# Kernel tuning notes

Hardware: AMD Instinct MI355X
Metric: run time of the kernel (lower is better)

## Reference

```python
import jax, jax.numpy as jnp
import numpy as np

BIN_SIZE = 128
DIST_MULT = 0.1
CLIP_LOW = 0.0
LN_EPS = 1e-6


def setup_inputs() -> dict:
    key = jax.random.key(0)
    ks = jax.random.split(key, 16)
    B, N, F, DD, MAXB = 8, 12800, 256, 128, 200
    s = 0.05  # ~TF random_normal initializer stddev
    inp = {}
    inp["x"] = jax.random.normal(ks[0], (B, N, F), jnp.float32)
    inp["msk"] = jax.random.uniform(ks[1], (B, N)) < 0.9
    # layernorm params
    inp["ln_g"] = jnp.ones((F,), jnp.float32)
    inp["ln_b"] = jnp.zeros((F,), jnp.float32)
    # ffn_dist: Dense(DD, elu) -> Dense(DD)
    inp["w1"] = jax.random.normal(ks[2], (F, DD), jnp.float32) * s
    inp["b1"] = jax.random.normal(ks[3], (DD,), jnp.float32) * s
    inp["w2"] = jax.random.normal(ks[4], (DD, DD), jnp.float32) * s
    inp["b2"] = jax.random.normal(ks[5], (DD,), jnp.float32) * s
    # LSH random rotations (non-trainable)
    inp["rot"] = jax.random.normal(ks[6], (DD, MAXB // 2), jnp.float32) * s
    # two GHConvDense layers (hidden=F -> output=F)
    inp["theta0"] = jax.random.normal(ks[7], (F, F), jnp.float32) * s
    inp["wh0"] = jax.random.normal(ks[8], (F, F), jnp.float32) * s
    inp["wt0"] = jax.random.normal(ks[9], (F, F), jnp.float32) * s
    inp["bt0"] = jax.random.normal(ks[10], (F,), jnp.float32) * s
    inp["theta1"] = jax.random.normal(ks[11], (F, F), jnp.float32) * s
    inp["wh1"] = jax.random.normal(ks[12], (F, F), jnp.float32) * s
    inp["wt1"] = jax.random.normal(ks[13], (F, F), jnp.float32) * s
    inp["bt1"] = jax.random.normal(ks[14], (F,), jnp.float32) * s
    return inp


def _ghconv(x, adj, mskf, theta, wh, wt, bt):
    # x: [B,nb,bs,F], adj: [B,nb,bs,bs], mskf: [B,nb,bs,1]
    deg = jnp.clip(jnp.sum(jnp.abs(adj), axis=-1), 0.0, 1000.0)  # [B,nb,bs]
    norm = ((deg + 1e-6) ** -0.5)[..., None] * mskf
    f_hom = jnp.matmul(x * mskf, theta) * mskf
    f_hom = jnp.matmul(adj, f_hom * norm) * norm
    f_het = jnp.matmul(x * mskf, wh)
    gate = jax.nn.sigmoid(jnp.matmul(x, wt) + bt)
    out = gate * f_hom + (1.0 - gate) * f_het
    return jax.nn.elu(out) * mskf


def _forward(x, msk, ln_g, ln_b, w1, b1, w2, b2, rot,
             theta0, wh0, wt0, bt0, theta1, wh1, wt1, bt1):
    B, N, F = x.shape
    nbins = N // BIN_SIZE
    # layernorm
    mu = jnp.mean(x, axis=-1, keepdims=True)
    var = jnp.mean((x - mu) ** 2, axis=-1, keepdims=True)
    xn = (x - mu) * jax.lax.rsqrt(var + LN_EPS) * ln_g + ln_b
    # ffn_dist
    xd = jnp.matmul(jax.nn.elu(jnp.matmul(xn, w1) + b1), w2) + b2  # [B,N,DD]
    # LSH binning
    mul = jnp.matmul(xd, rot[:, : nbins // 2])
    cmul = jnp.concatenate([mul, -mul], axis=-1)  # [B,N,nbins]
    bin_idx = jnp.argmax(cmul, axis=-1) + jnp.where(~msk, nbins - 1, 0)
    bins_split = jnp.argsort(bin_idx, axis=-1).reshape(B, nbins, BIN_SIZE)
    flat = bins_split.reshape(B, N)
    # gather into bins
    xd_b = jnp.take_along_axis(xd, flat[:, :, None], axis=1).reshape(B, nbins, BIN_SIZE, -1)
    x_b = jnp.take_along_axis(xn, flat[:, :, None], axis=1).reshape(B, nbins, BIN_SIZE, F)
    mskf = msk.astype(x.dtype)[:, :, None]
    m_b = jnp.take_along_axis(mskf, flat[:, :, None], axis=1).reshape(B, nbins, BIN_SIZE, 1)
    # pairwise gaussian kernel within bins
    na = jnp.sum(xd_b * xd_b, axis=-1)
    D2 = na[..., :, None] - 2.0 * jnp.einsum("bnie,bnje->bnij", xd_b, xd_b) + na[..., None, :]
    dm = jnp.exp(-DIST_MULT * jnp.sqrt(jnp.maximum(D2, 1e-6)))
    dm = jnp.clip(dm, CLIP_LOW, 1.0)
    m = m_b[..., 0]
    dm = dm * m[:, :, :, None] * m[:, :, None, :]
    # graph convs
    x_b = _ghconv(x_b, dm, m_b, theta0, wh0, wt0, bt0)
    x_b = _ghconv(x_b, dm, m_b, theta1, wh1, wt1, bt1)
    # reverse LSH scatter
    pts = x_b.reshape(B, N, F)
    x_enc = jnp.zeros((B, N, F), pts.dtype).at[jnp.arange(B)[:, None], flat].set(pts)
    return x_enc


def reference(x, msk, ln_g, ln_b, w1, b1, w2, b2, rot,
              theta0, wh0, wt0, bt0, theta1, wh1, wt1, bt1):
    return _forward(x, msk, ln_g, ln_b, w1, b1, w2, b2, rot,
                    theta0, wh0, wt0, bt0, theta1, wh1, wt1, bt1)
```

## Files before the change

kernel.cpp:

```cpp
#include <hip/hip_runtime.h>
#include <math.h>

#define BB 8
#define NN 12800
#define FF 256
#define DDIM 128
#define NBINS 100
#define BSIZE 128
#define NROT 50
#define NIDS 199
#define PTS (BB*NN)

#define OFF_OUT0 ((size_t)157286400)
#define OFF_DMB  ((size_t)209715200)
#define OFF_WB   ((size_t)235929600)
#define OFF_NORM ((size_t)236716032)
#define OFF_MF   ((size_t)237125632)
#define OFF_BIN  ((size_t)237535232)
#define OFF_FLAT ((size_t)237944832)
#define OFF_MSKI ((size_t)238354432)
#define OFF_HIST ((size_t)238764032)
#define OFF_OFFS ((size_t)239400832)
#define OFF_FLAG ((size_t)240037632)
#define OFF_CNT  ((size_t)240037696)
#define OFF_LIST ((size_t)240037760)
#define OFF_W1H  ((size_t)240447360)
#define OFF_W1L  ((size_t)240512896)
#define OFF_W2H  ((size_t)240578432)
#define OFF_W2L  ((size_t)240611200)
#define OFF_RH   ((size_t)240643968)
#define OFF_RL   ((size_t)240660352)
#define HISTBYTES (8*100*199*4)

using short8  = __attribute__((ext_vector_type(8))) short;
using floatx4 = __attribute__((ext_vector_type(4))) float;

__device__ __forceinline__ ushort f2b(float f) {
    unsigned u = __float_as_uint(f);
    unsigned r = (u + 0x7FFFu + ((u >> 16) & 1u)) >> 16;
    return (ushort)r;
}
__device__ __forceinline__ float b2f(ushort h) {
    return __uint_as_float(((unsigned)h) << 16);
}
__device__ __forceinline__ uint4 pack8(const ushort* o) {
    uint4 u;
    u.x = (unsigned)o[0] | ((unsigned)o[1] << 16);
    u.y = (unsigned)o[2] | ((unsigned)o[3] << 16);
    u.z = (unsigned)o[4] | ((unsigned)o[5] << 16);
    u.w = (unsigned)o[6] | ((unsigned)o[7] << 16);
    return u;
}

__global__ void k_maskflag(const int* mi, int* flag) {
    __shared__ int notInt, notFloat;
    if (threadIdx.x == 0) { notInt = 0; notFloat = 0; }
    __syncthreads();
    int v = mi[threadIdx.x];
    if (v != 0 && v != 1) atomicOr(&notInt, 1);
    if (v != 0 && v != 0x3F800000) atomicOr(&notFloat, 1);
    __syncthreads();
    if (threadIdx.x == 0) flag[0] = (!notInt) ? 0 : ((!notFloat) ? 2 : 1);
}

__global__ void k_masknorm(const void* msk, const int* flag, int* mski) {
    int i = blockIdx.x * blockDim.x + threadIdx.x;
    if (i >= PTS) return;
    int f = flag[0];
    int v;
    if (f == 0)      v = ((const int*)msk)[i] != 0;
    else if (f == 2) v = ((const float*)msk)[i] != 0.0f;
    else             v = ((const unsigned char*)msk)[i] != 0;
    mski[i] = v;
}

__global__ __launch_bounds__(256) void k_wprep(
    const float* s0, const float* s1, const float* s2,
    const float* s3, const float* s4, const float* s5,
    ushort* d0, ushort* d1, ushort* d2, ushort* d3, ushort* d4, ushort* d5)
{
    __shared__ float Ls[64 * 65];
    const float* src; ushort* dst;
    switch (blockIdx.y) {
        case 0: src = s0; dst = d0; break;
        case 1: src = s1; dst = d1; break;
        case 2: src = s2; dst = d2; break;
        case 3: src = s3; dst = d3; break;
        case 4: src = s4; dst = d4; break;
        default: src = s5; dst = d5; break;
    }
    int t = blockIdx.x;
    int kb = (t & 3) * 64, nb = (t >> 2) * 64;
    int tid = threadIdx.x;
    for (int q = 0; q < 4; ++q) {
        int g = q * 256 + tid;
        int kl = g >> 4, f4 = g & 15;
        float4 v = *(const float4*)(src + (size_t)(kb + kl) * 256 + nb + f4 * 4);
        Ls[kl * 65 + f4 * 4 + 0] = v.x;
        Ls[kl * 65 + f4 * 4 + 1] = v.y;
        Ls[kl * 65 + f4 * 4 + 2] = v.z;
        Ls[kl * 65 + f4 * 4 + 3] = v.w;
    }
    __syncthreads();
    for (int q = 0; q < 2; ++q) {
        int g = q * 256 + tid;
        int nl = g >> 3, wg = g & 7;
        ushort o[8];
        #pragma unroll
        for (int c = 0; c < 8; ++c) o[c] = f2b(Ls[(wg * 8 + c) * 65 + nl]);
        *(uint4*)(dst + (size_t)(nb + nl) * 256 + kb + wg * 8) = pack8(o);
    }
}

__global__ __launch_bounds__(256) void k_wsplit(const float* __restrict__ src, int K, int N,
                                               int srcN, int nvalid,
                                               ushort* __restrict__ dh, ushort* __restrict__ dl) {
    __shared__ float Ls[64 * 65];
    int tilesN = N >> 6;
    int kb = (blockIdx.x / tilesN) * 64, nb = (blockIdx.x % tilesN) * 64;
    int tid = threadIdx.x;
    for (int q = 0; q < 4; ++q) {
        int g = q * 256 + tid;
        int kl = g >> 4, c4 = (g & 15) * 4;
        #pragma unroll
        for (int j = 0; j < 4; ++j) {
            int n = nb + c4 + j;
            float v = (n < nvalid) ? src[(size_t)(kb + kl) * srcN + n] : 0.f;
            Ls[kl * 65 + c4 + j] = v;
        }
    }
    __syncthreads();
    for (int q = 0; q < 2; ++q) {
        int g = q * 256 + tid;
        int nl = g >> 3, wg = g & 7;
        ushort oh[8], ol[8];
        #pragma unroll
        for (int c = 0; c < 8; ++c) {
            float v = Ls[(wg * 8 + c) * 65 + nl];
            ushort h = f2b(v);
            oh[c] = h;
            ol[c] = f2b(v - b2f(h));
        }
        *(uint4*)(dh + (size_t)(nb + nl) * K + kb + wg * 8) = pack8(oh);
        *(uint4*)(dl + (size_t)(nb + nl) * K + kb + wg * 8) = pack8(ol);
    }
}

__device__ __forceinline__ void stage_async(const ushort* __restrict__ src, size_t pitch,
                                            const int* __restrict__ rowmap, int rowbase, size_t kbase,
                                            ushort* lds, int nrows, int tid) {
    int lane = tid & 63, wid = tid >> 6;
    int total = nrows * 8;
    for (int b0 = 0; b0 < total; b0 += 512) {
        int g = b0 + wid * 64 + lane;
        int row = g >> 3;
        int ck = (g & 7) ^ (row & 7);
        size_t srow = rowmap ? (size_t)rowmap[rowbase + row] : (size_t)(rowbase + row);
        const ushort* gp = src + srow * pitch + kbase + ck * 8;
        ushort* lp = lds + (size_t)(b0 + wid * 64) * 8;
        __builtin_amdgcn_global_load_lds(
            (const __attribute__((address_space(1))) unsigned int*)gp,
            (__attribute__((address_space(3))) unsigned int*)lp, 16, 0, 0);
    }
}

__device__ __forceinline__ short8 frag_ld(const ushort* lds, int row, int kc, int lane) {
    int w0 = (kc * 16 + ((lane >> 4) << 2)) ^ ((row & 7) << 2);
    return *(const short8*)((const char*)lds + row * 128 + w0 * 4);
}

__global__ __launch_bounds__(512, 4) void k_stage1(
    const float* __restrict__ x, const float* __restrict__ g, const float* __restrict__ be,
    const float* __restrict__ b1, const float* __restrict__ b2,
    const ushort* __restrict__ w1h, const ushort* __restrict__ w1l,
    const ushort* __restrict__ w2h, const ushort* __restrict__ w2l,
    const ushort* __restrict__ rth, const ushort* __restrict__ rtl,
    const int* __restrict__ mski,
    ushort* __restrict__ xn_out, float* __restrict__ xd_out, int* __restrict__ bin_out,
    int* __restrict__ fixlist, int* __restrict__ fixcnt)
{
    __shared__ ushort lXh[4 * 2048];
    __shared__ ushort lXl[4 * 2048];
    __shared__ ushort lWh[8192];
    __shared__ ushort lWl[8192];
    int tid = threadIdx.x, lane = tid & 63, wid = tid >> 6;
    int base = blockIdx.x * 32;
    int l15 = lane & 15;
    int r4 = (lane >> 4) * 4;

    stage_async(w1h, 256, nullptr, 0, 0, lWh, 128, tid);
    stage_async(w1l, 256, nullptr, 0, 0, lWl, 128, tid);

    {
        int row = tid >> 4, sub = tid & 15;
        const float* xr = x + (size_t)(base + row) * FF + sub * 16;
        float v[16];
        float s = 0.f;
        #pragma unroll
        for (int q = 0; q < 4; ++q) {
            float4 f = *(const float4*)(xr + q * 4);
            v[q*4+0] = f.x; v[q*4+1] = f.y; v[q*4+2] = f.z; v[q*4+3] = f.w;
            s += f.x + f.y + f.z + f.w;
        }
        s += __shfl_xor(s, 1, 16); s += __shfl_xor(s, 2, 16);
        s += __shfl_xor(s, 4, 16); s += __shfl_xor(s, 8, 16);
        float mu = s * (1.f / 256.f);
        float s2 = 0.f;
        #pragma unroll
        for (int q = 0; q < 16; ++q) { float d = v[q] - mu; s2 += d * d; }
        s2 += __shfl_xor(s2, 1, 16); s2 += __shfl_xor(s2, 2, 16);
        s2 += __shfl_xor(s2, 4, 16); s2 += __shfl_xor(s2, 8, 16);
        float rs = 1.0f / sqrtf(s2 * (1.f / 256.f) + 1e-6f);
        ushort* xo = xn_out + (size_t)(base + row) * FF + sub * 16;
        #pragma unroll
        for (int j = 0; j < 2; ++j) {
            int i0 = sub * 16 + j * 8;
            float4 g0 = *(const float4*)(g + i0);
            float4 g1 = *(const float4*)(g + i0 + 4);
            float4 e0 = *(const float4*)(be + i0);
            float4 e1 = *(const float4*)(be + i0 + 4);
            float gv[8] = {g0.x,g0.y,g0.z,g0.w,g1.x,g1.y,g1.z,g1.w};
            float ev[8] = {e0.x,e0.y,e0.z,e0.w,e1.x,e1.y,e1.z,e1.w};
            ushort hh[8], ll[8];
            #pragma unroll
            for (int c = 0; c < 8; ++c) {
                float xv = (v[j*8+c] - mu) * rs * gv[c] + ev[c];
                ushort h = f2b(xv);
                hh[c] = h;
                ll[c] = f2b(xv - b2f(h));
            }
            uint4 uh = pack8(hh), ul = pack8(ll);
            *(uint4*)(xo + j * 8) = uh;
            int kb = i0 >> 6;
            int wg = (i0 & 63) >> 3;
            int w0 = (wg * 4) ^ ((row & 7) << 2);
            *(uint4*)((char*)lXh + kb * 4096 + row * 128 + w0 * 4) = uh;
            *(uint4*)((char*)lXl + kb * 4096 + row * 128 + w0 * 4) = ul;
        }
    }
    __syncthreads();

    int mg = wid >> 2, ng = wid & 3;
    int wm = mg * 16, wn = ng * 32;
    floatx4 zf = {0.f, 0.f, 0.f, 0.f};

    floatx4 acc[2];
    acc[0] = zf; acc[1] = zf;
    for (int kb = 0; kb < 4; ++kb) {
        #pragma unroll
        for (int kc = 0; kc < 2; ++kc) {
            short8 ah, al, bh[2], bl[2];
            ah = frag_ld(lXh + kb * 2048, wm + l15, kc, lane);
            al = frag_ld(lXl + kb * 2048, wm + l15, kc, lane);
            #pragma unroll
            for (int n = 0; n < 2; n++) {
                bh[n] = frag_ld(lWh, wn + n * 16 + l15, kc, lane);
                bl[n] = frag_ld(lWl, wn + n * 16 + l15, kc, lane);
            }
            #pragma unroll
            for (int n = 0; n < 2; n++) {
                acc[n] = __builtin_amdgcn_mfma_f32_16x16x32_bf16(ah, bh[n], acc[n], 0, 0, 0);
                acc[n] = __builtin_amdgcn_mfma_f32_16x16x32_bf16(ah, bl[n], acc[n], 0, 0, 0);
                acc[n] = __builtin_amdgcn_mfma_f32_16x16x32_bf16(al, bh[n], acc[n], 0, 0, 0);
            }
        }
        __syncthreads();
        if (kb < 3) {
            stage_async(w1h, 256, nullptr, 0, (size_t)(kb + 1) * 64, lWh, 128, tid);
            stage_async(w1l, 256, nullptr, 0, (size_t)(kb + 1) * 64, lWl, 128, tid);
            __syncthreads();
        }
    }
    stage_async(w2h, 128, nullptr, 0, 0, lWh, 128, tid);
    stage_async(w2l, 128, nullptr, 0, 0, lWl, 128, tid);
    {
        #pragma unroll
        for (int n = 0; n < 2; n++) {
            int cg = wn + n * 16 + l15;
            float b1v = b1[cg];
            int slab = cg >> 6, c64 = cg & 63;
            int wg = c64 >> 3, e = c64 & 7;
            #pragma unroll
            for (int i = 0; i < 4; i++) {
                int r = wm + r4 + i;
                float hv = acc[n][i] + b1v;
                hv = (hv > 0.f) ? hv : expm1f(hv);
                ushort h = f2b(hv);
                int w0 = (wg * 4) ^ ((r & 7) << 2);
                int idx = slab * 2048 + r * 64 + w0 * 2 + e;
                lXh[idx] = h;
                lXl[idx] = f2b(hv - b2f(h));
            }
        }
    }
    __syncthreads();

    floatx4 acc2[2];
    acc2[0] = zf; acc2[1] = zf;
    for (int kb = 0; kb < 2; ++kb) {
        #pragma unroll
        for (int kc = 0; kc < 2; ++kc) {
            short8 ah, al, bh[2], bl[2];
            ah = frag_ld(lXh + kb * 2048, wm + l15, kc, lane);
            al = frag_ld(lXl + kb * 2048, wm + l15, kc, lane);
            #pragma unroll
            for (int n = 0; n < 2; n++) {
                bh[n] = frag_ld(lWh, wn + n * 16 + l15, kc, lane);
                bl[n] = frag_ld(lWl, wn + n * 16 + l15, kc, lane);
            }
            #pragma unroll
            for (int n = 0; n < 2; n++) {
                acc2[n] = __builtin_amdgcn_mfma_f32_16x16x32_bf16(ah, bh[n], acc2[n], 0, 0, 0);
                acc2[n] = __builtin_amdgcn_mfma_f32_16x16x32_bf16(ah, bl[n], acc2[n], 0, 0, 0);
                acc2[n] = __builtin_amdgcn_mfma_f32_16x16x32_bf16(al, bh[n], acc2[n], 0, 0, 0);
            }
        }
        __syncthreads();
        if (kb == 0) {
            stage_async(w2h, 128, nullptr, 0, 64, lWh, 128, tid);
            stage_async(w2l, 128, nullptr, 0, 64, lWl, 128, tid);
            __syncthreads();
        }
    }
    stage_async(rth, 128, nullptr, 0, 0, lWh, 64, tid);
    stage_async(rtl, 128, nullptr, 0, 0, lWl, 64, tid);
    stage_async(rth, 128, nullptr, 0, 64, lWh + 4096, 64, tid);
    stage_async(rtl, 128, nullptr, 0, 64, lWl + 4096, 64, tid);
    {
        #pragma unroll
        for (int n = 0; n < 2; n++) {
            int cg = wn + n * 16 + l15;
            float b2v = b2[cg];
            int slab = 2 + (cg >> 6), c64 = cg & 63;
            int wg = c64 >> 3, e = c64 & 7;
            #pragma unroll
            for (int i = 0; i < 4; i++) {
                int r = wm + r4 + i;
                float xv = acc2[n][i] + b2v;
                xd_out[(size_t)(base + r) * DDIM + cg] = xv;
                ushort h = f2b(xv);
                int w0 = (wg * 4) ^ ((r & 7) << 2);
                int idx = slab * 2048 + r * 64 + w0 * 2 + e;
                lXh[idx] = h;
                lXl[idx] = f2b(xv - b2f(h));
            }
        }
    }
    __syncthreads();

    floatx4 acc3 = zf;
    int wn3 = ng * 16;
    for (int kb = 0; kb < 2; ++kb) {
        #pragma unroll
        for (int kc = 0; kc < 2; ++kc) {
            short8 ah, al, bh, bl;
            ah = frag_ld(lXh + (2 + kb) * 2048, wm + l15, kc, lane);
            al = frag_ld(lXl + (2 + kb) * 2048, wm + l15, kc, lane);
            bh = frag_ld(lWh + kb * 4096, wn3 + l15, kc, lane);
            bl = frag_ld(lWl + kb * 4096, wn3 + l15, kc, lane);
            acc3 = __builtin_amdgcn_mfma_f32_16x16x32_bf16(ah, bh, acc3, 0, 0, 0);
            acc3 = __builtin_amdgcn_mfma_f32_16x16x32_bf16(ah, bl, acc3, 0, 0, 0);
            acc3 = __builtin_amdgcn_mfma_f32_16x16x32_bf16(al, bh, acc3, 0, 0, 0);
        }
    }
    __syncthreads();
    float* lMul = (float*)lXh;
    {
        #pragma unroll
        for (int i = 0; i < 4; i++) {
            int r = wm + r4 + i;
            lMul[r * 65 + wn3 + l15] = acc3[i];
        }
    }
    __syncthreads();

    {
        int p = tid >> 4, q = tid & 15;
        float v1 = -1e30f, v2 = -1e30f; int i1 = 1 << 29;
        #pragma unroll
        for (int j = 0; j < 4; ++j) {
            int c = q * 4 + j;
            if (c < 50) {
                float m = lMul[p * 65 + c];
                float wv, lv; int wi, li;
                if (m >= 0.f) { wv = m; wi = c; lv = -m; li = 50 + c; }
                else          { wv = -m; wi = 50 + c; lv = m; li = c; }
                if (wv > v1 || (wv == v1 && wi < i1)) { v2 = v1; v1 = wv; i1 = wi; }
                else if (wv > v2) v2 = wv;
                if (lv > v1 || (lv == v1 && li < i1)) { v2 = v1; v1 = lv; i1 = li; }
                else if (lv > v2) v2 = lv;
            }
        }
        #pragma unroll
        for (int off = 1; off < 16; off <<= 1) {
            float o1 = __shfl_xor(v1, off, 16);
            int   oi = __shfl_xor(i1, off, 16);
            float o2 = __shfl_xor(v2, off, 16);
            bool take = (o1 > v1) || (o1 == v1 && oi < i1);
            float small = take ? v1 : o1;
            if (take) { v1 = o1; i1 = oi; }
            v2 = fmaxf(fmaxf(v2, o2), small);
        }
        if (q == 0) {
            int pt = base + p;
            bin_out[pt] = i1 + (mski[pt] ? 0 : (NBINS - 1));
            float tau = 3e-4f + 1.5e-3f * v1;
            if (v1 - v2 < tau) {
                int pos = atomicAdd(fixcnt, 1);
                fixlist[pos] = pt;
            }
        }
    }
}

__global__ __launch_bounds__(64) void k_fixup(
    const float* __restrict__ x, const float* __restrict__ g, const float* __restrict__ be,
    const float* __restrict__ w1, const float* __restrict__ b1,
    const float* __restrict__ w2, const float* __restrict__ b2,
    const float* __restrict__ rot, const int* __restrict__ mski,
    const int* __restrict__ fixlist, const int* __restrict__ fixcnt,
    int* __restrict__ bin_out)
{
    __shared__ double xn_s[256];
    __shared__ double h_s[128];
    __shared__ double xd_s[128];
    int lane = threadIdx.x;
    int n = fixcnt[0];
    for (int e = blockIdx.x; e < n; e += gridDim.x) {
        int pt = fixlist[e];
        const float* xr = x + (size_t)pt * FF;
        double s = 0.0, xv[4];
        #pragma unroll
        for (int q = 0; q < 4; q++) { xv[q] = (double)xr[lane + q * 64]; s += xv[q]; }
        #pragma unroll
        for (int off = 1; off < 64; off <<= 1) s += __shfl_xor(s, off, 64);
        double mu = s * (1.0 / 256.0);
        double s2 = 0.0;
        #pragma unroll
        for (int q = 0; q < 4; q++) { double d = xv[q] - mu; s2 += d * d; }
        #pragma unroll
        for (int off = 1; off < 64; off <<= 1) s2 += __shfl_xor(s2, off, 64);
        double rs = 1.0 / sqrt(s2 * (1.0 / 256.0) + 1e-6);
        #pragma unroll
        for (int q = 0; q < 4; q++) {
            int i = lane + q * 64;
            xn_s[i] = (xv[q] - mu) * rs * (double)g[i] + (double)be[i];
        }
        __syncthreads();
        #pragma unroll
        for (int q = 0; q < 2; q++) {
            int j = lane + q * 64;
            double a0 = 0.0, a1 = 0.0;
            for (int k = 0; k < FF; k += 2) {
                a0 += xn_s[k] * (double)w1[k * DDIM + j];
                a1 += xn_s[k + 1] * (double)w1[(k + 1) * DDIM + j];
            }
            double a = (double)b1[j] + a0 + a1;
            h_s[j] = (a > 0.0) ? a : expm1(a);
        }
        __syncthreads();
        #pragma unroll
        for (int q = 0; q < 2; q++) {
            int j = lane + q * 64;
            double a0 = 0.0, a1 = 0.0;
            for (int k = 0; k < DDIM; k += 2) {
                a0 += h_s[k] * (double)w2[k * DDIM + j];
                a1 += h_s[k + 1] * (double)w2[(k + 1) * DDIM + j];
            }
            xd_s[j] = (double)b2[j] + a0 + a1;
        }
        __syncthreads();
        double v; int idx;
        if (lane < NROT) {
            double m = 0.0;
            for (int k = 0; k < DDIM; k++) m += xd_s[k] * (double)rot[k * 100 + lane];
            if (m >= 0.0) { v = m; idx = lane; } else { v = -m; idx = 50 + lane; }
        } else { v = -1e300; idx = 1 << 29; }
        #pragma unroll
        for (int off = 1; off < 64; off <<= 1) {
            double ov = __shfl_xor(v, off, 64);
            int oi = __shfl_xor(idx, off, 64);
            if (ov > v || (ov == v && oi < idx)) { v = ov; idx = oi; }
        }
        if (lane == 0) bin_out[pt] = idx + (mski[pt] ? 0 : (NBINS - 1));
        __syncthreads();
    }
}

__global__ void k_count(const int* __restrict__ bin, int* __restrict__ hist) {
    int c = blockIdx.x % 100, b = blockIdx.x / 100;
    int t = threadIdx.x;
    int v = bin[b * NN + c * BSIZE + t];
    atomicAdd(&hist[(b * 100 + c) * NIDS + v], 1);
}

__global__ void k_offsets(const int* __restrict__ hist, int* __restrict__ offs) {
    __shared__ int tot[NIDS];
    __shared__ int start[NIDS];
    int b = blockIdx.x, v = threadIdx.x;
    if (v < NIDS) {
        int s = 0;
        for (int c = 0; c < 100; c++) s += hist[(b * 100 + c) * NIDS + v];
        tot[v] = s;
    }
    __syncthreads();
    if (threadIdx.x == 0) {
        int run = 0;
        for (int i = 0; i < NIDS; i++) { start[i] = run; run += tot[i]; }
    }
    __syncthreads();
    if (v < NIDS) {
        int run = start[v];
        for (int c = 0; c < 100; c++) {
            offs[(b * 100 + c) * NIDS + v] = run;
            run += hist[(b * 100 + c) * NIDS + v];
        }
    }
}

__global__ void k_scatter(const int* __restrict__ bin, const int* __restrict__ offs,
                          const int* __restrict__ mski, int* __restrict__ flat,
                          float* __restrict__ mf) {
    __shared__ int sv[BSIZE];
    int c = blockIdx.x % 100, b = blockIdx.x / 100;
    int t = threadIdx.x;
    int n = c * BSIZE + t;
    int v = bin[b * NN + n];
    sv[t] = v;
    __syncthreads();
    int rank = 0;
    for (int u = 0; u < t; u++) rank += (sv[u] == v);
    int r = offs[(b * 100 + c) * NIDS + v] + rank;
    flat[b * NN + r] = b * NN + n;
    mf[b * NN + r] = mski[b * NN + n] ? 1.0f : 0.0f;
}

__global__ __launch_bounds__(256) void k_dm(const float* __restrict__ xd, const int* __restrict__ flat,
                                            const float* __restrict__ mf, ushort* __restrict__ dmb,
                                            float* __restrict__ norm) {
    __shared__ float Xs[128 * 64];
    __shared__ float na[128];
    __shared__ float ml[128];
    __shared__ float ps[128 * 16];
    int g = blockIdx.x, tid = threadIdx.x;
    int tx = tid & 15, ty = tid >> 4;
    int rowbase = g * 128;
    if (tid < 128) ml[tid] = mf[rowbase + tid];
    float acc[8][8];
    #pragma unroll
    for (int i = 0; i < 8; i++)
        #pragma unroll
        for (int j = 0; j < 8; j++) acc[i][j] = 0.f;
    float nap[8];
    #pragma unroll
    for (int j = 0; j < 8; j++) nap[j] = 0.f;

    for (int kh = 0; kh < 2; ++kh) {
        __syncthreads();
        for (int q = 0; q < 8; ++q) {
            int gg = q * 256 + tid;
            int row = gg >> 4, f4 = gg & 15;
            int srow = flat[rowbase + row];
            float4 v = *(const float4*)(xd + (size_t)srow * DDIM + kh * 64 + f4 * 4);
            int f4s = f4 ^ ((row >> 3) & 7);
            *(float4*)(Xs + row * 64 + f4s * 4) = v;
        }
        __syncthreads();
        for (int k4 = 0; k4 < 16; ++k4) {
            int sa = (k4 ^ (ty & 7)) << 2;
            int sb = (k4 ^ (tx & 7)) << 2;
            float4 av[8], bv[8];
            #pragma unroll
            for (int i = 0; i < 8; i++) av[i] = *(const float4*)(Xs + (ty * 8 + i) * 64 + sa);
            #pragma unroll
            for (int j = 0; j < 8; j++) bv[j] = *(const float4*)(Xs + (tx * 8 + j) * 64 + sb);
            if (ty == 0) {
                #pragma unroll
                for (int j = 0; j < 8; j++)
                    nap[j] += bv[j].x * bv[j].x + bv[j].y * bv[j].y + bv[j].z * bv[j].z + bv[j].w * bv[j].w;
            }
            #pragma unroll
            for (int i = 0; i < 8; i++)
                #pragma unroll
                for (int j = 0; j < 8; j++)
                    acc[i][j] += av[i].x * bv[j].x + av[i].y * bv[j].y + av[i].z * bv[j].z + av[i].w * bv[j].w;
        }
    }
    if (ty == 0) {
        #pragma unroll
        for (int j = 0; j < 8; j++) na[tx * 8 + j] = nap[j];
    }
    __syncthreads();
    #pragma unroll
    for (int i = 0; i < 8; ++i) {
        int r = ty * 8 + i;
        float nai = na[r], mi = ml[r];
        float rs = 0.f;
        ushort o[8];
        #pragma unroll
        for (int j = 0; j < 8; ++j) {
            int c = tx * 8 + j;
            float D2 = nai - 2.f * acc[i][j] + na[c];
            float dv = expf(-0.1f * sqrtf(fmaxf(D2, 1e-6f)));
            dv *= mi * ml[c];
            rs += dv;
            o[j] = f2b(dv);
        }
        *(uint4*)(dmb + (size_t)g * 16384 + r * 128 + tx * 8) = pack8(o);
        ps[r * 16 + tx] = rs;
    }
    __syncthreads();
    if (tid < 128) {
        float deg = 0.f;
        for (int t2 = 0; t2 < 16; ++t2) deg += ps[tid * 16 + t2];
        deg = fminf(deg, 1000.0f);
        float nv = 1.0f / sqrtf(deg + 1e-6f);
        norm[rowbase + tid] = nv * ml[tid];
    }
}

template<int LAYER>
__global__ __launch_bounds__(512, 4) void k_layer(
    const ushort* __restrict__ A, const int* __restrict__ rowmap,
    const ushort* __restrict__ ThT, const ushort* __restrict__ WhT, const ushort* __restrict__ WtT,
    const float* __restrict__ bt, const ushort* __restrict__ dmb,
    const float* __restrict__ norm, const float* __restrict__ mf,
    ushort* __restrict__ outb, float* __restrict__ outf, const int* __restrict__ flatscat)
{
    __shared__ char smem[81920];
    ushort* lAbuf = (ushort*)smem;
    ushort* lB    = (ushort*)(smem + 32768);
    ushort* lT    = (ushort*)smem;
    ushort* ldm   = (ushort*)(smem + 32768);

    int tid = threadIdx.x, lane = tid & 63, wid = tid >> 6;
    int bid = blockIdx.x;
    int grp = bid >> 5, within = bid & 31;
    int nh = within >> 3, g = grp * 8 + (within & 7);
    int rowbase = g * 128, nbase = nh * 64;
    int l15 = lane & 15;
    int r4 = (lane >> 4) * 4;
    int wm = (wid >> 1) * 32, wn = (wid & 1) * 32;
    const ushort* dmg = dmb + (size_t)g * 16384;
    floatx4 zf = {0.f, 0.f, 0.f, 0.f};

    stage_async(A, 256, rowmap, rowbase, 0, lAbuf, 128, tid);
    stage_async(ThT, 256, nullptr, nbase, 0, lB + 0 * 4096, 64, tid);
    stage_async(WhT, 256, nullptr, nbase, 0, lB + 2 * 4096, 64, tid);
    stage_async(WtT, 256, nullptr, nbase, 0, lB + 4 * 4096, 64, tid);
    __syncthreads();

    floatx4 accT[2][2], accH[2][2], accG[2][2];
    #pragma unroll
    for (int m = 0; m < 2; m++)
        #pragma unroll
        for (int n = 0; n < 2; n++) { accT[m][n] = zf; accH[m][n] = zf; accG[m][n] = zf; }
    for (int kb = 0; kb < 4; ++kb) {
        if (kb < 3) {
            int pp = (kb + 1) & 1;
            stage_async(A, 256, rowmap, rowbase, (size_t)(kb + 1) * 64, lAbuf + pp * 8192, 128, tid);
            stage_async(ThT, 256, nullptr, nbase, (size_t)(kb + 1) * 64, lB + (0 + pp) * 4096, 64, tid);
            stage_async(WhT, 256, nullptr, nbase, (size_t)(kb + 1) * 64, lB + (2 + pp) * 4096, 64, tid);
            stage_async(WtT, 256, nullptr, nbase, (size_t)(kb + 1) * 64, lB + (4 + pp) * 4096, 64, tid);
        }
        const ushort* lA = lAbuf + (kb & 1) * 8192;
        const ushort* sTh = lB + (0 + (kb & 1)) * 4096;
        const ushort* sWh = lB + (2 + (kb & 1)) * 4096;
        const ushort* sWt = lB + (4 + (kb & 1)) * 4096;
        #pragma unroll
        for (int kc = 0; kc < 2; ++kc) {
            short8 a[2], bt_[2], bh_[2], bg_[2];
            #pragma unroll
            for (int m = 0; m < 2; m++) a[m] = frag_ld(lA, wm + m * 16 + l15, kc, lane);
            #pragma unroll
            for (int n = 0; n < 2; n++) {
                bt_[n] = frag_ld(sTh, wn + n * 16 + l15, kc, lane);
                bh_[n] = frag_ld(sWh, wn + n * 16 + l15, kc, lane);
                bg_[n] = frag_ld(sWt, wn + n * 16 + l15, kc, lane);
            }
            #pragma unroll
            for (int m = 0; m < 2; m++)
                #pragma unroll
                for (int n = 0; n < 2; n++) {
                    accT[m][n] = __builtin_amdgcn_mfma_f32_16x16x32_bf16(a[m], bt_[n], accT[m][n], 0, 0, 0);
                    accH[m][n] = __builtin_amdgcn_mfma_f32_16x16x32_bf16(a[m], bh_[n], accH[m][n], 0, 0, 0);
                    accG[m][n] = __builtin_amdgcn_mfma_f32_16x16x32_bf16(a[m], bg_[n], accG[m][n], 0, 0, 0);
                }
        }
        __syncthreads();
    }

    stage_async(dmg, 128, nullptr, 0, 0, ldm, 128, tid);
    stage_async(dmg, 128, nullptr, 0, 64, ldm + 8192, 128, tid);

    {
        #pragma unroll
        for (int m = 0; m < 2; m++) {
            float4 nv = *(const float4*)(norm + rowbase + wm + m * 16 + r4);
            float nvv[4] = {nv.x, nv.y, nv.z, nv.w};
            int jloc0 = wm + m * 16 + r4;
            int jb = jloc0 >> 6, jj = jloc0 & 63;
            #pragma unroll
            for (int n = 0; n < 2; n++) {
                int cloc = wn + n * 16 + l15;
                char* bp = (char*)(lT + jb * 4096) + cloc * 128;
                int cx = (cloc & 7) << 2;
                ushort t0 = f2b(accT[m][n][0] * nvv[0]);
                ushort t1 = f2b(accT[m][n][1] * nvv[1]);
                ushort t2 = f2b(accT[m][n][2] * nvv[2]);
                ushort t3 = f2b(accT[m][n][3] * nvv[3]);
                *(unsigned*)(bp + ((((jj >> 1) + 0) ^ cx) << 2)) = (unsigned)t0 | ((unsigned)t1 << 16);
                *(unsigned*)(bp + ((((jj >> 1) + 1) ^ cx) << 2)) = (unsigned)t2 | ((unsigned)t3 << 16);
            }
        }
    }
    __syncthreads();

    floatx4 accFH[2][2];
    #pragma unroll
    for (int m = 0; m < 2; m++) { accFH[m][0] = zf; accFH[m][1] = zf; }
    for (int kb = 0; kb < 2; ++kb) {
        #pragma unroll
        for (int kc = 0; kc < 2; ++kc) {
            short8 a[2], b[2];
            #pragma unroll
            for (int m = 0; m < 2; m++) a[m] = frag_ld(ldm + kb * 8192, wm + m * 16 + l15, kc, lane);
            #pragma unroll
            for (int n = 0; n < 2; n++) b[n] = frag_ld(lT + kb * 4096, wn + n * 16 + l15, kc, lane);
            #pragma unroll
            for (int m = 0; m < 2; m++)
                #pragma unroll
                for (int n = 0; n < 2; n++)
                    accFH[m][n] = __builtin_amdgcn_mfma_f32_16x16x32_bf16(a[m], b[n], accFH[m][n], 0, 0, 0);
        }
    }
    __syncthreads();

    for (int m = 0; m < 2; m++) {
        int r0l = wm + m * 16 + r4;
        int r0g = rowbase + r0l;
        float4 mv = *(const float4*)(mf + r0g);
        float4 nv = *(const float4*)(norm + r0g);
        float mvv[4] = {mv.x, mv.y, mv.z, mv.w};
        float nvv[4] = {nv.x, nv.y, nv.z, nv.w};
        float vals[2][4];
        #pragma unroll
        for (int n = 0; n < 2; n++) {
            int cg = nbase + wn + n * 16 + l15;
            float btc = bt[cg];
            #pragma unroll
            for (int i = 0; i < 4; i++) {
                float gate = 1.f / (1.f + expf(-(accG[m][n][i] + btc)));
                float fh = accFH[m][n][i] * nvv[i];
                float het = mvv[i] * accH[m][n][i];
                float o = gate * fh + (1.f - gate) * het;
                o = (o > 0.f) ? o : expm1f(o);
                vals[n][i] = o * mvv[i];
            }
        }
        if (LAYER == 0) {
            ushort* Ls = (ushort*)smem;
            int bbase = wid * 512;
            #pragma unroll
            for (int n = 0; n < 2; n++)
                #pragma unroll
                for (int i = 0; i < 4; i++)
                    Ls[bbase + (r4 + i) * 32 + n * 16 + l15] = f2b(vals[n][i]);
            __builtin_amdgcn_s_waitcnt(0);
            #pragma unroll
            for (int it = 0; it < 2; ++it) {
                int lr = (lane >> 3) + it * 8;
                int lc4 = (lane & 7) * 4;
                ushort4 tv = *(const ushort4*)(Ls + bbase + lr * 32 + lc4);
                int rg = rowbase + wm + m * 16 + lr;
                *(ushort4*)(outb + (size_t)rg * 256 + nbase + wn + lc4) = tv;
            }
        } else {
            float* Ls = (float*)smem;
            int bbase = wid * 512;
            #pragma unroll
            for (int n = 0; n < 2; n++)
                #pragma unroll
                for (int i = 0; i < 4; i++)
                    Ls[bbase + (r4 + i) * 32 + n * 16 + l15] = vals[n][i];
            __builtin_amdgcn_s_waitcnt(0);
            #pragma unroll
            for (int it = 0; it < 2; ++it) {
                int lr = (lane >> 3) + it * 8;
                int lc4 = (lane & 7) * 4;
                float4 tv = *(const float4*)(Ls + bbase + lr * 32 + lc4);
                int rg = rowbase + wm + m * 16 + lr;
                int dst = flatscat[rg];
                *(float4*)(outf + (size_t)dst * 256 + nbase + wn + lc4) = tv;
            }
        }
    }
}

extern "C" void kernel_launch(void* const* d_in, const int* in_sizes, int n_in,
                              void* d_out, int out_size, void* d_ws, size_t ws_size,
                              hipStream_t stream) {
    const float* x    = (const float*)d_in[0];
    const void*  msk  = d_in[1];
    const float* ln_g = (const float*)d_in[2];
    const float* ln_b = (const float*)d_in[3];
    const float* w1   = (const float*)d_in[4];
    const float* b1   = (const float*)d_in[5];
    const float* w2   = (const float*)d_in[6];
    const float* b2   = (const float*)d_in[7];
    const float* rot  = (const float*)d_in[8];
    const float* th0  = (const float*)d_in[9];
    const float* wh0  = (const float*)d_in[10];
    const float* wt0  = (const float*)d_in[11];
    const float* bt0  = (const float*)d_in[12];
    const float* th1  = (const float*)d_in[13];
    const float* wh1  = (const float*)d_in[14];
    const float* wt1  = (const float*)d_in[15];
    const float* bt1  = (const float*)d_in[16];

    char* ws = (char*)d_ws;
    ushort* out0 = (ushort*)(ws + OFF_OUT0);
    ushort* dmb  = (ushort*)(ws + OFF_DMB);
    ushort* wb   = (ushort*)(ws + OFF_WB);
    ushort* wbth0 = wb + 0 * 65536;
    ushort* wbwh0 = wb + 1 * 65536;
    ushort* wbwt0 = wb + 2 * 65536;
    ushort* wbth1 = wb + 3 * 65536;
    ushort* wbwh1 = wb + 4 * 65536;
    ushort* wbwt1 = wb + 5 * 65536;
    float* norm = (float*)(ws + OFF_NORM);
    float* mf   = (float*)(ws + OFF_MF);
    int*   bin  = (int*)(ws + OFF_BIN);
    int*   flat = (int*)(ws + OFF_FLAT);
    int*   mski = (int*)(ws + OFF_MSKI);
    int*   hist = (int*)(ws + OFF_HIST);
    int*   offs = (int*)(ws + OFF_OFFS);
    int*   flag = (int*)(ws + OFF_FLAG);
    int*   fixcnt = (int*)(ws + OFF_CNT);
    int*   fixlist = (int*)(ws + OFF_LIST);
    ushort* w1h = (ushort*)(ws + OFF_W1H);
    ushort* w1l = (ushort*)(ws + OFF_W1L);
    ushort* w2h = (ushort*)(ws + OFF_W2H);
    ushort* w2l = (ushort*)(ws + OFF_W2L);
    ushort* rth = (ushort*)(ws + OFF_RH);
    ushort* rtl = (ushort*)(ws + OFF_RL);
    float*  xd  = (float*)d_out;
    ushort* xnb = (ushort*)((char*)d_out + (size_t)PTS * DDIM * 4);

    hipMemsetAsync(hist, 0, HISTBYTES, stream);
    hipMemsetAsync(fixcnt, 0, 4, stream);
    k_maskflag<<<1, 256, 0, stream>>>((const int*)msk, flag);
    k_masknorm<<<PTS / 256, 256, 0, stream>>>(msk, flag, mski);
    k_wprep<<<dim3(16, 6), 256, 0, stream>>>(th0, wh0, wt0, th1, wh1, wt1,
                                             wbth0, wbwh0, wbwt0, wbth1, wbwh1, wbwt1);
    k_wsplit<<<8, 256, 0, stream>>>(w1, 256, 128, 128, 128, w1h, w1l);
    k_wsplit<<<4, 256, 0, stream>>>(w2, 128, 128, 128, 128, w2h, w2l);
    k_wsplit<<<2, 256, 0, stream>>>(rot, 128, 64, 100, 50, rth, rtl);
    k_stage1<<<PTS / 32, 512, 0, stream>>>(x, ln_g, ln_b, b1, b2,
                                           w1h, w1l, w2h, w2l, rth, rtl, mski,
                                           xnb, xd, bin, fixlist, fixcnt);
    k_fixup<<<4096, 64, 0, stream>>>(x, ln_g, ln_b, w1, b1, w2, b2, rot, mski,
                                     fixlist, fixcnt, bin);
    k_count<<<800, 128, 0, stream>>>(bin, hist);
    k_offsets<<<8, 256, 0, stream>>>(hist, offs);
    k_scatter<<<800, 128, 0, stream>>>(bin, offs, mski, flat, mf);
    k_dm<<<800, 256, 0, stream>>>(xd, flat, mf, dmb, norm);
    k_layer<0><<<3200, 512, 0, stream>>>(xnb, flat, wbth0, wbwh0, wbwt0, bt0,
                                         dmb, norm, mf, out0, nullptr, nullptr);
    k_layer<1><<<3200, 512, 0, stream>>>(out0, nullptr, wbth1, wbwh1, wbwt1, bt1,
                                         dmb, norm, mf, nullptr, (float*)d_out, flat);
}
```

Baseline: 439.8 us.

## Compute pairwise bin distances with split-bf16 MFMA instead of fp32 FMA

The pairwise Gram matrix inside each bin moves from a scalar fp32 outer-product loop to MFMA bf16 instructions using a hi/lo split (three MFMAs per tile) for near-fp32 accuracy. To feed it, stage1 now writes the distance features as separate hi and lo bf16 arrays instead of fp32, and the gather uses async global-to-LDS loads. The output tile is staged through padded LDS and written out in coalesced chunks, with the row-sum reduction done by shuffles. Dropping the small low*low term introduces slight precision loss in the distances.

```diff
diff --git a/kernel.cpp b/kernel.cpp
--- a/kernel.cpp
+++ b/kernel.cpp
@@ -176,8 +176,8 @@
     const ushort* __restrict__ w2h, const ushort* __restrict__ w2l,
     const ushort* __restrict__ rth, const ushort* __restrict__ rtl,
     const int* __restrict__ mski,
-    ushort* __restrict__ xn_out, float* __restrict__ xd_out, int* __restrict__ bin_out,
-    int* __restrict__ fixlist, int* __restrict__ fixcnt)
+    ushort* __restrict__ xn_out, ushort* __restrict__ xdh_out, ushort* __restrict__ xdl_out,
+    int* __restrict__ bin_out, int* __restrict__ fixlist, int* __restrict__ fixcnt)
 {
     __shared__ ushort lXh[4 * 2048];
     __shared__ ushort lXl[4 * 2048];
@@ -337,12 +337,15 @@
             for (int i = 0; i < 4; i++) {
                 int r = wm + r4 + i;
                 float xv = acc2[n][i] + b2v;
-                xd_out[(size_t)(base + r) * DDIM + cg] = xv;
                 ushort h = f2b(xv);
+                ushort lo = f2b(xv - b2f(h));
+                size_t go = (size_t)(base + r) * DDIM + cg;
+                xdh_out[go] = h;
+                xdl_out[go] = lo;
                 int w0 = (wg * 4) ^ ((r & 7) << 2);
                 int idx = slab * 2048 + r * 64 + w0 * 2 + e;
                 lXh[idx] = h;
-                lXl[idx] = f2b(xv - b2f(h));
+                lXl[idx] = lo;
             }
         }
     }
@@ -535,87 +538,125 @@
     mf[b * NN + r] = mski[b * NN + n] ? 1.0f : 0.0f;
 }
 
-__global__ __launch_bounds__(256) void k_dm(const float* __restrict__ xd, const int* __restrict__ flat,
-                                            const float* __restrict__ mf, ushort* __restrict__ dmb,
-                                            float* __restrict__ norm) {
-    __shared__ float Xs[128 * 64];
+__global__ __launch_bounds__(512, 4) void k_dm(const ushort* __restrict__ xdh, const ushort* __restrict__ xdl,
+                                               const int* __restrict__ flat, const float* __restrict__ mf,
+                                               ushort* __restrict__ dmb, float* __restrict__ norm) {
+    __shared__ ushort lX[32768];
     __shared__ float na[128];
     __shared__ float ml[128];
-    __shared__ float ps[128 * 16];
-    int g = blockIdx.x, tid = threadIdx.x;
-    int tx = tid & 15, ty = tid >> 4;
+    __shared__ float ps[512];
+    int tid = threadIdx.x, lane = tid & 63, wid = tid >> 6;
+    int g = blockIdx.x;
     int rowbase = g * 128;
+    int l15 = lane & 15;
+    int r4 = (lane >> 4) * 4;
+    int mg = wid >> 2, ng = wid & 3;
+    int wm = mg * 64, wn = ng * 32;
+    floatx4 zf = {0.f, 0.f, 0.f, 0.f};
+
+    stage_async(xdh, 128, flat, rowbase, 0, lX, 128, tid);
+    stage_async(xdh, 128, flat, rowbase, 64, lX + 8192, 128, tid);
+    stage_async(xdl, 128, flat, rowbase, 0, lX + 16384, 128, tid);
+    stage_async(xdl, 128, flat, rowbase, 64, lX + 24576, 128, tid);
     if (tid < 128) ml[tid] = mf[rowbase + tid];
-    float acc[8][8];
+    __syncthreads();
+
+    {
+        int row = tid >> 2, part = tid & 3;
+        float s = 0.f;
+        #pragma unroll
+        for (int kb = 0; kb < 2; ++kb) {
+            const ushort* ph = lX + kb * 8192 + row * 64 + part * 16;
+            #pragma unroll
+            for (int q = 0; q < 2; ++q) {
+                uint4 uh = *(const uint4*)(ph + q * 8);
+                uint4 ul = *(const uint4*)(ph + 16384 + q * 8);
+                const unsigned* wh_ = (const unsigned*)&uh;
+                const unsigned* wl_ = (const unsigned*)&ul;
+                #pragma unroll
+                for (int w = 0; w < 4; ++w) {
+                    float x0 = b2f((ushort)(wh_[w] & 0xFFFFu)) + b2f((ushort)(wl_[w] & 0xFFFFu));
+                    float x1 = b2f((ushort)(wh_[w] >> 16)) + b2f((ushort)(wl_[w] >> 16));
+                    s = fmaf(x0, x0, s);
+                    s = fmaf(x1, x1, s);
+                }
+            }
+        }
+        s += __shfl_xor(s, 1, 4);
+        s += __shfl_xor(s, 2, 4);
+        if (part == 0) na[row] = s;
+    }
+
+    floatx4 acc[4][2];
     #pragma unroll
-    for (int i = 0; i < 8; i++)
-        #pragma unroll
-        for (int j = 0; j < 8; j++) acc[i][j] = 0.f;
-    float nap[8];
+    for (int m = 0; m < 4; m++) { acc[m][0] = zf; acc[m][1] = zf; }
+    for (int kb = 0; kb < 2; ++kb) {
+        #pragma unroll
+        for (int kc = 0; kc < 2; ++kc) {
+            short8 ah[4], al[4], bh[2], bl[2];
+            #pragma unroll
+            for (int m = 0; m < 4; m++) {
+                ah[m] = frag_ld(lX + kb * 8192, wm + m * 16 + l15, kc, lane);
+                al[m] = frag_ld(lX + 16384 + kb * 8192, wm + m * 16 + l15, kc, lane);
+            }
+            #pragma unroll
+            for (int n = 0; n < 2; n++) {
+                bh[n] = frag_ld(lX + kb * 8192, wn + n * 16 + l15, kc, lane);
+                bl[n] = frag_ld(lX + 16384 + kb * 8192, wn + n * 16 + l15, kc, lane);
+            }
+            #pragma unroll
+            for (int m = 0; m < 4; m++)
+                #pragma unroll
+                for (int n = 0; n < 2; n++) {
+                    acc[m][n] = __builtin_amdgcn_mfma_f32_16x16x32_bf16(ah[m], bh[n], acc[m][n], 0, 0, 0);
+                    acc[m][n] = __builtin_amdgcn_mfma_f32_16x16x32_bf16(ah[m], bl[n], acc[m][n], 0, 0, 0);
+                    acc[m][n] = __builtin_amdgcn_mfma_f32_16x16x32_bf16(al[m], bh[n], acc[m][n], 0, 0, 0);
+                }
+        }
+    }
+    __syncthreads();
+
+    ushort* Ls = lX;
+    for (int m = 0; m < 4; ++m) {
+        int r0 = wm + m * 16 + r4;
+        float rs[4] = {0.f, 0.f, 0.f, 0.f};
+        #pragma unroll
+        for (int n = 0; n < 2; ++n) {
+            int c = wn + n * 16 + l15;
+            float nac = na[c], mlc = ml[c];
+            #pragma unroll
+            for (int i = 0; i < 4; ++i) {
+                int r = r0 + i;
+                float D2 = na[r] - 2.f * acc[m][n][i] + nac;
+                float dv = expf(-0.1f * sqrtf(fmaxf(D2, 1e-6f)));
+                dv *= ml[r] * mlc;
+                rs[i] += dv;
+                Ls[r * 136 + c] = f2b(dv);
+            }
+        }
+        #pragma unroll
+        for (int off = 1; off < 16; off <<= 1) {
+            #pragma unroll
+            for (int i = 0; i < 4; ++i) rs[i] += __shfl_xor(rs[i], off, 16);
+        }
+        if (l15 == 0) {
+            #pragma unroll
+            for (int i = 0; i < 4; ++i) ps[(r0 + i) * 4 + ng] = rs[i];
+        }
+    }
+    __syncthreads();
+
     #pragma unroll
-    for (int j = 0; j < 8; j++) nap[j] = 0.f;
-
-    for (int kh = 0; kh < 2; ++kh) {
-        __syncthreads();
-        for (int q = 0; q < 8; ++q) {
-            int gg = q * 256 + tid;
-            int row = gg >> 4, f4 = gg & 15;
-            int srow = flat[rowbase + row];
-            float4 v = *(const float4*)(xd + (size_t)srow * DDIM + kh * 64 + f4 * 4);
-            int f4s = f4 ^ ((row >> 3) & 7);
-            *(float4*)(Xs + row * 64 + f4s * 4) = v;
-        }
-        __syncthreads();
-        for (int k4 = 0; k4 < 16; ++k4) {
-            int sa = (k4 ^ (ty & 7)) << 2;
-            int sb = (k4 ^ (tx & 7)) << 2;
-            float4 av[8], bv[8];
-            #pragma unroll
-            for (int i = 0; i < 8; i++) av[i] = *(const float4*)(Xs + (ty * 8 + i) * 64 + sa);
-            #pragma unroll
-            for (int j = 0; j < 8; j++) bv[j] = *(const float4*)(Xs + (tx * 8 + j) * 64 + sb);
-            if (ty == 0) {
-                #pragma unroll
-                for (int j = 0; j < 8; j++)
-                    nap[j] += bv[j].x * bv[j].x + bv[j].y * bv[j].y + bv[j].z * bv[j].z + bv[j].w * bv[j].w;
-            }
-            #pragma unroll
-            for (int i = 0; i < 8; i++)
-                #pragma unroll
-                for (int j = 0; j < 8; j++)
-                    acc[i][j] += av[i].x * bv[j].x + av[i].y * bv[j].y + av[i].z * bv[j].z + av[i].w * bv[j].w;
-        }
-    }
-    if (ty == 0) {
-        #pragma unroll
-        for (int j = 0; j < 8; j++) na[tx * 8 + j] = nap[j];
-    }
-    __syncthreads();
-    #pragma unroll
-    for (int i = 0; i < 8; ++i) {
-        int r = ty * 8 + i;
-        float nai = na[r], mi = ml[r];
-        float rs = 0.f;
-        ushort o[8];
-        #pragma unroll
-        for (int j = 0; j < 8; ++j) {
-            int c = tx * 8 + j;
-            float D2 = nai - 2.f * acc[i][j] + na[c];
-            float dv = expf(-0.1f * sqrtf(fmaxf(D2, 1e-6f)));
-            dv *= mi * ml[c];
-            rs += dv;
-            o[j] = f2b(dv);
-        }
-        *(uint4*)(dmb + (size_t)g * 16384 + r * 128 + tx * 8) = pack8(o);
-        ps[r * 16 + tx] = rs;
-    }
-    __syncthreads();
+    for (int it = 0; it < 4; ++it) {
+        int gi = it * 512 + tid;
+        int row = gi >> 4, ch = gi & 15;
+        uint4 v = *(const uint4*)(Ls + row * 136 + ch * 8);
+        *(uint4*)(dmb + (size_t)g * 16384 + row * 128 + ch * 8) = v;
+    }
     if (tid < 128) {
-        float deg = 0.f;
-        for (int t2 = 0; t2 < 16; ++t2) deg += ps[tid * 16 + t2];
+        float deg = ps[tid * 4 + 0] + ps[tid * 4 + 1] + ps[tid * 4 + 2] + ps[tid * 4 + 3];
         deg = fminf(deg, 1000.0f);
-        float nv = 1.0f / sqrtf(deg + 1e-6f);
-        norm[rowbase + tid] = nv * ml[tid];
+        norm[rowbase + tid] = (1.0f / sqrtf(deg + 1e-6f)) * ml[tid];
     }
 }
 
@@ -844,7 +885,8 @@
     ushort* w2l = (ushort*)(ws + OFF_W2L);
     ushort* rth = (ushort*)(ws + OFF_RH);
     ushort* rtl = (ushort*)(ws + OFF_RL);
-    float*  xd  = (float*)d_out;
+    ushort* xdh = (ushort*)d_out;
+    ushort* xdl = xdh + (size_t)PTS * DDIM;
     ushort* xnb = (ushort*)((char*)d_out + (size_t)PTS * DDIM * 4);
 
     hipMemsetAsync(hist, 0, HISTBYTES, stream);
@@ -858,13 +900,13 @@
     k_wsplit<<<2, 256, 0, stream>>>(rot, 128, 64, 100, 50, rth, rtl);
     k_stage1<<<PTS / 32, 512, 0, stream>>>(x, ln_g, ln_b, b1, b2,
                                            w1h, w1l, w2h, w2l, rth, rtl, mski,
-                                           xnb, xd, bin, fixlist, fixcnt);
+                                           xnb, xdh, xdl, bin, fixlist, fixcnt);
     k_fixup<<<4096, 64, 0, stream>>>(x, ln_g, ln_b, w1, b1, w2, b2, rot, mski,
                                      fixlist, fixcnt, bin);
     k_count<<<800, 128, 0, stream>>>(bin, hist);
     k_offsets<<<8, 256, 0, stream>>>(hist, offs);
     k_scatter<<<800, 128, 0, stream>>>(bin, offs, mski, flat, mf);
-    k_dm<<<800, 256, 0, stream>>>(xd, flat, mf, dmb, norm);
+    k_dm<<<800, 512, 0, stream>>>(xdh, xdl, flat, mf, dmb, norm);
     k_layer<0><<<3200, 512, 0, stream>>>(xnb, flat, wbth0, wbwh0, wbwt0, bt0,
                                          dmb, norm, mf, out0, nullptr, nullptr);
     k_layer<1><<<3200, 512, 0, stream>>>(out0, nullptr, wbth1, wbwh1, wbwt1, bt1,
```

New measurement: 389.7 us (median of 3 runs). 1.13x faster.
